# Kernel tuning notes

Measured on AMD Instinct MI355X. Metric: run time of the kernel, lower is better.

The kernel has to match this reference:

```python
import jax, jax.numpy as jnp
import numpy as np

SIGMA = 1.0
RADIUS = 3          # Gaussian kernel radius -> kernel size 7
TAU = 1.0
ITERATIONS = 20
EPS = 1e-6


def _gauss_kernel_1d(sigma: float, radius: int) -> jnp.ndarray:
    x = jnp.arange(-radius, radius + 1, dtype=jnp.float32)
    k = jnp.exp(-0.5 * (x / sigma) ** 2)
    return k / k.sum()


def _smooth(v: jnp.ndarray, k1d: jnp.ndarray) -> jnp.ndarray:
    """Separable Gaussian smoothing of a (1, C, D, H, W) field, 'same' padding."""
    C = v.shape[1]
    r = (k1d.size - 1) // 2
    for ax in range(3):
        shape = [1, 1, 1]
        shape[ax] = k1d.size
        ker = jnp.tile(k1d.reshape((1, 1) + tuple(shape)), (C, 1, 1, 1, 1))
        pad = [(r, r) if i == ax else (0, 0) for i in range(3)]
        v = jax.lax.conv_general_dilated(
            v, ker, window_strides=(1, 1, 1), padding=pad,
            dimension_numbers=('NCDHW', 'OIDHW', 'NCDHW'),
            feature_group_count=C)
    return v


def _warp(image: jnp.ndarray, disp: jnp.ndarray) -> jnp.ndarray:
    """Trilinear warp of (1,1,D,H,W) image by voxel displacement (1,3,D,H,W)."""
    D, H, W = image.shape[2:]
    gd, gh, gw = jnp.meshgrid(
        jnp.arange(D, dtype=disp.dtype),
        jnp.arange(H, dtype=disp.dtype),
        jnp.arange(W, dtype=disp.dtype), indexing='ij')
    coords = [gd + disp[0, 0], gh + disp[0, 1], gw + disp[0, 2]]
    warped = jax.scipy.ndimage.map_coordinates(image[0, 0], coords, order=1, mode='nearest')
    return warped[None, None]


def _spatial_gradient(img: jnp.ndarray) -> jnp.ndarray:
    # img: (D, H, W) -> (3, D, H, W), central differences
    return jnp.stack(jnp.gradient(img))


def _demon_forces_dual(warped, fixed, fixed_grad):
    # warped/fixed: (1,1,D,H,W); dual gradient = mean of moving/fixed gradients
    diff = (warped - fixed)[0, 0]                      # (D,H,W)
    g = 0.5 * (_spatial_gradient(warped[0, 0]) + fixed_grad)  # (3,D,H,W)
    denom = (g ** 2).sum(axis=0) + diff ** 2           # (D,H,W)
    f = jnp.where(denom > EPS, diff * g / denom, 0.0)  # (3,D,H,W)
    return f[None]                                     # (1,3,D,H,W)


def setup_inputs() -> dict:
    key = jax.random.key(0)
    k1, k2 = jax.random.split(key)
    shape = (1, 1, 128, 128, 128)
    moving_image = jax.random.uniform(k1, shape, dtype=jnp.float32)
    fixed_image = jax.random.uniform(k2, shape, dtype=jnp.float32)
    return {"moving_image": moving_image, "fixed_image": fixed_image}


def reference(moving_image, fixed_image):
    kernel = _gauss_kernel_1d(SIGMA, RADIUS)
    fixed_grad = _spatial_gradient(fixed_image[0, 0])
    vf0 = jnp.zeros((1, 3) + moving_image.shape[2:], dtype=moving_image.dtype)

    def step(vf, _):
        warped = _warp(moving_image, vf)
        forces = _demon_forces_dual(warped, fixed_image, fixed_grad)
        vf = _smooth(vf + TAU * forces, kernel)
        return vf, None

    vf, _ = jax.lax.scan(step, vf0, None, length=ITERATIONS)
    return vf
```

## Files before the change

### kernel.cpp

```cpp
#include <hip/hip_runtime.h>
#include <hip/hip_cooperative_groups.h>

namespace cg = cooperative_groups;

static constexpr int DIM = 128;
static constexpr int N = DIM * DIM * DIM;
static constexpr int ITERS = 20;
static constexpr float EPS = 1e-6f;

#define W0 0.39905028f
#define W1 0.24203624f
#define W2 0.05400559f
#define W3 0.00443305f

__device__ __forceinline__ int clamp_i(int v, int lo, int hi) {
    return min(max(v, lo), hi);
}

#define ROWS 22
#define SSTR 132
#define SC(c, r) ((((c) * ROWS) + (r)) * SSTR)
#define LDS_FLOATS (3 * ROWS * SSTR)

__device__ __forceinline__ void forces_phase(const float* __restrict__ wpd,
                                             const float* __restrict__ fix,
                                             const float* __restrict__ vf,
                                             float* __restrict__ u2,
                                             float* S, bool first, int b) {
    int z  = b >> 3;
    int y0 = (b & 7) << 4;

    for (int e = threadIdx.x; e < ROWS * 32; e += 256) {
        int x4 = e & 31;
        int r  = e >> 5;
        int gy = y0 + r - 3;
        float4 rz = make_float4(0, 0, 0, 0);
        float4 ry = make_float4(0, 0, 0, 0);
        float4 rx = make_float4(0, 0, 0, 0);
        if (gy >= 0 && gy < 128) {
            int idx = (z << 14) + (gy << 7) + (x4 << 2);
            int xb = x4 << 2;

            float4 wc4 = *(const float4*)(wpd + idx);
            float4 fc4 = *(const float4*)(fix + idx);

            int iyp = (gy < 127) ? idx + 128   : idx;
            int iym = (gy > 0)   ? idx - 128   : idx;
            int izp = (z < 127)  ? idx + 16384 : idx;
            int izm = (z > 0)    ? idx - 16384 : idx;

            float4 wyp = *(const float4*)(wpd + iyp), wym = *(const float4*)(wpd + iym);
            float4 wzp = *(const float4*)(wpd + izp), wzm = *(const float4*)(wpd + izm);
            float4 fyp = *(const float4*)(fix + iyp), fym = *(const float4*)(fix + iym);
            float4 fzp = *(const float4*)(fix + izp), fzm = *(const float4*)(fix + izm);

            float wl = __shfl_up(wc4.w, 1);
            float wr = __shfl_down(wc4.x, 1);
            float fl = __shfl_up(fc4.w, 1);
            float fr = __shfl_down(fc4.x, 1);

            float wcv[4] = {wc4.x, wc4.y, wc4.z, wc4.w};
            float fcv[4] = {fc4.x, fc4.y, fc4.z, fc4.w};
            float wypv[4] = {wyp.x, wyp.y, wyp.z, wyp.w};
            float wymv[4] = {wym.x, wym.y, wym.z, wym.w};
            float wzpv[4] = {wzp.x, wzp.y, wzp.z, wzp.w};
            float wzmv[4] = {wzm.x, wzm.y, wzm.z, wzm.w};
            float fypv[4] = {fyp.x, fyp.y, fyp.z, fyp.w};
            float fymv[4] = {fym.x, fym.y, fym.z, fym.w};
            float fzpv[4] = {fzp.x, fzp.y, fzp.z, fzp.w};
            float fzmv[4] = {fzm.x, fzm.y, fzm.z, fzm.w};

            float4 vz4 = first ? make_float4(0, 0, 0, 0) : *(const float4*)(vf + idx);
            float4 vy4 = first ? make_float4(0, 0, 0, 0) : *(const float4*)(vf + N + idx);
            float4 vx4 = first ? make_float4(0, 0, 0, 0) : *(const float4*)(vf + 2 * N + idx);
            float vzv[4] = {vz4.x, vz4.y, vz4.z, vz4.w};
            float vyv[4] = {vy4.x, vy4.y, vy4.z, vy4.w};
            float vxv[4] = {vx4.x, vx4.y, vx4.z, vx4.w};

            float ozv[4], oyv[4], oxv[4];
#pragma unroll
            for (int i = 0; i < 4; ++i) {
                float wc = wcv[i], fc = fcv[i];
                float diff = wc - fc;

                float gwz = (z == 0)   ? (wzpv[i] - wc)
                          : (z == 127) ? (wc - wzmv[i])
                          : 0.5f * (wzpv[i] - wzmv[i]);
                float gfz = (z == 0)   ? (fzpv[i] - fc)
                          : (z == 127) ? (fc - fzmv[i])
                          : 0.5f * (fzpv[i] - fzmv[i]);
                float grz = 0.5f * (gwz + gfz);

                float gwy = (gy == 0)   ? (wypv[i] - wc)
                          : (gy == 127) ? (wc - wymv[i])
                          : 0.5f * (wypv[i] - wymv[i]);
                float gfy = (gy == 0)   ? (fypv[i] - fc)
                          : (gy == 127) ? (fc - fymv[i])
                          : 0.5f * (fypv[i] - fymv[i]);
                float gry = 0.5f * (gwy + gfy);

                float wleft  = (i == 0) ? wl : wcv[i - 1];
                float wright = (i == 3) ? wr : wcv[i + 1];
                float fleft  = (i == 0) ? fl : fcv[i - 1];
                float fright = (i == 3) ? fr : fcv[i + 1];
                int xi = xb + i;
                float gwx = (xi == 0)   ? (wright - wc)
                          : (xi == 127) ? (wc - wleft)
                          : 0.5f * (wright - wleft);
                float gfx = (xi == 0)   ? (fright - fc)
                          : (xi == 127) ? (fc - fleft)
                          : 0.5f * (fright - fleft);
                float grx = 0.5f * (gwx + gfx);

                float denom = grz * grz + gry * gry + grx * grx + diff * diff;
                float s = (denom > EPS) ? (diff / denom) : 0.0f;
                ozv[i] = vzv[i] + s * grz;
                oyv[i] = vyv[i] + s * gry;
                oxv[i] = vxv[i] + s * grx;
            }
            rz = make_float4(ozv[0], ozv[1], ozv[2], ozv[3]);
            ry = make_float4(oyv[0], oyv[1], oyv[2], oyv[3]);
            rx = make_float4(oxv[0], oxv[1], oxv[2], oxv[3]);
        }

        float4 vch[3] = {rz, ry, rx};
#pragma unroll
        for (int c = 0; c < 3; ++c) {
            float4 v0 = vch[c];
            float4 m1, p1;
            m1.x = __shfl_up(v0.x, 1);  m1.y = __shfl_up(v0.y, 1);
            m1.z = __shfl_up(v0.z, 1);  m1.w = __shfl_up(v0.w, 1);
            p1.x = __shfl_down(v0.x, 1); p1.y = __shfl_down(v0.y, 1);
            p1.z = __shfl_down(v0.z, 1); p1.w = __shfl_down(v0.w, 1);
            if (x4 == 0)  m1 = make_float4(0, 0, 0, 0);
            if (x4 == 31) p1 = make_float4(0, 0, 0, 0);
            float w[12] = {m1.x, m1.y, m1.z, m1.w,
                           v0.x, v0.y, v0.z, v0.w,
                           p1.x, p1.y, p1.z, p1.w};
            float o[4];
#pragma unroll
            for (int i = 0; i < 4; ++i) {
                o[i] = W3 * (w[i + 1] + w[i + 7]) + W2 * (w[i + 2] + w[i + 6])
                     + W1 * (w[i + 3] + w[i + 5]) + W0 * w[i + 4];
            }
            *(float4*)(S + SC(c, r) + (x4 << 2)) = make_float4(o[0], o[1], o[2], o[3]);
        }
    }
    __syncthreads();

    for (int e = threadIdx.x; e < 16 * 32 * 3; e += 256) {
        int x4 = e & 31;
        int t2 = e >> 5;
        int y  = t2 & 15;
        int c  = t2 >> 4;
        const float* base = S + SC(c, y) + (x4 << 2);
        float4 v0 = *(const float4*)(base);
        float4 v1 = *(const float4*)(base + 1 * SSTR);
        float4 v2 = *(const float4*)(base + 2 * SSTR);
        float4 v3 = *(const float4*)(base + 3 * SSTR);
        float4 v4 = *(const float4*)(base + 4 * SSTR);
        float4 v5 = *(const float4*)(base + 5 * SSTR);
        float4 v6 = *(const float4*)(base + 6 * SSTR);
        float4 acc;
        acc.x = W3 * (v0.x + v6.x) + W2 * (v1.x + v5.x) + W1 * (v2.x + v4.x) + W0 * v3.x;
        acc.y = W3 * (v0.y + v6.y) + W2 * (v1.y + v5.y) + W1 * (v2.y + v4.y) + W0 * v3.y;
        acc.z = W3 * (v0.z + v6.z) + W2 * (v1.z + v5.z) + W1 * (v2.z + v4.z) + W0 * v3.z;
        acc.w = W3 * (v0.w + v6.w) + W2 * (v1.w + v5.w) + W1 * (v2.w + v4.w) + W0 * v3.w;
        *(float4*)(u2 + (size_t)c * N + ((size_t)z << 14) + ((y0 + y) << 7) + (x4 << 2)) = acc;
    }
}

__device__ __forceinline__ void zblur_phase(const float* __restrict__ u2,
                                            const float* __restrict__ mov,
                                            float* __restrict__ vf,
                                            float* __restrict__ warped,
                                            bool do_warp, int b) {
    int k  = b & 7;
    int j  = b >> 3;
    int lb = ((j & 15) << 6) + (k << 3) + (j >> 4);
    int g  = lb * 256 + threadIdx.x;
    int col = g & 16383;
    int zc  = g >> 14;
    int z0  = zc << 3;
    int x = col & 127, y = col >> 7;

    float bz[3][8];
#pragma unroll
    for (int c = 0; c < 3; ++c) {
        const float* inp = u2 + (size_t)c * N + col;
        float win[14];
#pragma unroll
        for (int i = 0; i < 14; ++i) {
            int zz = z0 - 3 + i;
            win[i] = (zz >= 0 && zz < 128) ? inp[(size_t)zz << 14] : 0.0f;
        }
#pragma unroll
        for (int k8 = 0; k8 < 8; ++k8) {
            bz[c][k8] = W3 * (win[k8] + win[k8 + 6]) + W2 * (win[k8 + 1] + win[k8 + 5])
                      + W1 * (win[k8 + 2] + win[k8 + 4]) + W0 * win[k8 + 3];
        }
        float* outp = vf + (size_t)c * N + col;
#pragma unroll
        for (int k8 = 0; k8 < 8; ++k8)
            outp[(size_t)(z0 + k8) << 14] = bz[c][k8];
    }

    if (do_warp) {
        for (int k8 = 0; k8 < 8; ++k8) {
            int z = z0 + k8;
            float cz = (float)z + bz[0][k8];
            float cy = (float)y + bz[1][k8];
            float cx = (float)x + bz[2][k8];

            float flz = floorf(cz), fly = floorf(cy), flx = floorf(cx);
            float fz = cz - flz, fy = cy - fly, fx = cx - flx;

            int zi = (int)flz, yi = (int)fly, xi = (int)flx;
            int z0c = clamp_i(zi, 0, DIM - 1), z1c = clamp_i(zi + 1, 0, DIM - 1);
            int y0c = clamp_i(yi, 0, DIM - 1), y1c = clamp_i(yi + 1, 0, DIM - 1);
            int x0c = clamp_i(xi, 0, DIM - 1), x1c = clamp_i(xi + 1, 0, DIM - 1);

            int b00 = (z0c << 14) + (y0c << 7);
            int b01 = (z0c << 14) + (y1c << 7);
            int b10 = (z1c << 14) + (y0c << 7);
            int b11 = (z1c << 14) + (y1c << 7);

            float v000 = mov[b00 + x0c], v001 = mov[b00 + x1c];
            float v010 = mov[b01 + x0c], v011 = mov[b01 + x1c];
            float v100 = mov[b10 + x0c], v101 = mov[b10 + x1c];
            float v110 = mov[b11 + x0c], v111 = mov[b11 + x1c];

            float c00 = v000 + fx * (v001 - v000);
            float c01 = v010 + fx * (v011 - v010);
            float c10 = v100 + fx * (v101 - v100);
            float c11 = v110 + fx * (v111 - v110);
            float c0 = c00 + fy * (c01 - c00);
            float c1 = c10 + fy * (c11 - c10);
            warped[((size_t)z << 14) + col] = c0 + fz * (c1 - c0);
        }
    }
}

__device__ __forceinline__ void wait_ge(unsigned int* c, unsigned int target) {
    while (__hip_atomic_load(c, __ATOMIC_ACQUIRE, __HIP_MEMORY_SCOPE_AGENT) < target)
        __builtin_amdgcn_s_sleep(1);
}

__global__ __launch_bounds__(256, 4) void demons_persistent(const float* mov,
                                                            const float* fix,
                                                            float* vf,
                                                            float* warped,
                                                            float* u2,
                                                            unsigned int* cnt) {
    cg::grid_group grid = cg::this_grid();
    __shared__ float S[LDS_FLOATS];
    int b = blockIdx.x;
    int s = b & 7;
    unsigned int* cntA = cnt;
    unsigned int* cntB = cnt + 8;

    if (b == 0 && threadIdx.x < 16) cnt[threadIdx.x] = 0u;
    grid.sync();

    for (int it = 0; it < ITERS; ++it) {
        bool first = (it == 0);
        if (!first) {
            if (threadIdx.x == 0) {
                unsigned int tgt = (unsigned int)it * 128u;
                if (s > 0) wait_ge(&cntB[s - 1], tgt);
                wait_ge(&cntB[s], tgt);
                if (s < 7) wait_ge(&cntB[s + 1], tgt);
            }
            __syncthreads();
        }
        forces_phase(first ? mov : warped, fix, vf, u2, S, first, b);
        __syncthreads();
        if (threadIdx.x == 0) {
            __hip_atomic_fetch_add(&cntA[s], 1u, __ATOMIC_RELEASE, __HIP_MEMORY_SCOPE_AGENT);
            unsigned int tgt = (unsigned int)(it + 1) * 128u;
            if (s > 0) wait_ge(&cntA[s - 1], tgt);
            wait_ge(&cntA[s], tgt);
            if (s < 7) wait_ge(&cntA[s + 1], tgt);
        }
        __syncthreads();
        zblur_phase(u2, mov, vf, warped, it < ITERS - 1, b);
        if (it < ITERS - 1) {
            __syncthreads();
            if (threadIdx.x == 0)
                __hip_atomic_fetch_add(&cntB[s], 1u, __ATOMIC_RELEASE, __HIP_MEMORY_SCOPE_AGENT);
        }
    }
}

template <bool FIRST>
__global__ __launch_bounds__(256, 4) void forces_xy_kernel(const float* __restrict__ wpd,
                                                           const float* __restrict__ fix,
                                                           const float* __restrict__ vf,
                                                           float* __restrict__ u2) {
    __shared__ float S[LDS_FLOATS];
    forces_phase(wpd, fix, vf, u2, S, FIRST, blockIdx.x);
}

template <bool DO_WARP>
__global__ __launch_bounds__(256, 4) void zblur_warp_kernel(const float* __restrict__ u2,
                                                            const float* __restrict__ mov,
                                                            float* __restrict__ vf,
                                                            float* __restrict__ warped) {
    zblur_phase(u2, mov, vf, warped, DO_WARP, blockIdx.x);
}

extern "C" void kernel_launch(void* const* d_in, const int* in_sizes, int n_in,
                              void* d_out, int out_size, void* d_ws, size_t ws_size,
                              hipStream_t stream) {
    const float* mov = (const float*)d_in[0];
    const float* fix = (const float*)d_in[1];
    float* vf = (float*)d_out;
    float* ws = (float*)d_ws;
    float* warped = ws;
    float* u2     = ws + (size_t)N;
    unsigned int* cnt = (unsigned int*)(ws + (size_t)4 * N);

    const int BLK = 256;
    const int GRID = 1024;

    static int coop_ok = -1;
    if (coop_ok < 0) {
        int dev = 0;
        (void)hipGetDevice(&dev);
        int coop = 0;
        (void)hipDeviceGetAttribute(&coop, hipDeviceAttributeCooperativeLaunch, dev);
        int ncu = 0;
        (void)hipDeviceGetAttribute(&ncu, hipDeviceAttributeMultiprocessorCount, dev);
        int occ = 0;
        (void)hipOccupancyMaxActiveBlocksPerMultiprocessor(&occ, demons_persistent, BLK, 0);
        coop_ok = (coop && (long long)occ * ncu >= GRID &&
                   ws_size >= (size_t)4 * N * sizeof(float) + 64) ? 1 : 0;
    }

    if (coop_ok) {
        void* args[] = {(void*)&mov, (void*)&fix, (void*)&vf, (void*)&warped,
                        (void*)&u2, (void*)&cnt};
        (void)hipLaunchCooperativeKernel(demons_persistent, dim3(GRID), dim3(BLK),
                                         args, 0, stream);
    } else {
        forces_xy_kernel<true><<<GRID, BLK, 0, stream>>>(mov, fix, nullptr, u2);
        zblur_warp_kernel<true><<<GRID, BLK, 0, stream>>>(u2, mov, vf, warped);
        for (int it = 1; it < ITERS - 1; ++it) {
            forces_xy_kernel<false><<<GRID, BLK, 0, stream>>>(warped, fix, vf, u2);
            zblur_warp_kernel<true><<<GRID, BLK, 0, stream>>>(u2, mov, vf, warped);
        }
        forces_xy_kernel<false><<<GRID, BLK, 0, stream>>>(warped, fix, vf, u2);
        zblur_warp_kernel<false><<<GRID, BLK, 0, stream>>>(u2, mov, vf, warped);
    }
}
```

Before: 766.9 us.

## Replace per-slab counters with fine-grained per-block dependency flags in persistent kernel

Swaps the coarse per-slab counters, each of which waited for all 128 blocks of a slab and its neighbours, for per-block flags indexed by slab and z. Each block now waits only on the neighbouring blocks whose z range its stencil or warp actually reads, with many threads polling in parallel. The aim is to cut barrier stalls and let waves of blocks proceed without full slab synchronisation. In exchange it adds more atomic polling traffic and depends on the hand-computed z dependency ranges being correct. It also adds a fallback to separate kernels when the cooperative launch fails.

Result: no change. 763.9 us (-0.4%).

```diff
diff --git a/kernel.cpp b/kernel.cpp
--- a/kernel.cpp
+++ b/kernel.cpp
@@ -251,43 +251,65 @@
                                                             float* vf,
                                                             float* warped,
                                                             float* u2,
-                                                            unsigned int* cnt) {
+                                                            unsigned int* flags) {
     cg::grid_group grid = cg::this_grid();
     __shared__ float S[LDS_FLOATS];
     int b = blockIdx.x;
     int s = b & 7;
-    unsigned int* cntA = cnt;
-    unsigned int* cntB = cnt + 8;
-
-    if (b == 0 && threadIdx.x < 16) cnt[threadIdx.x] = 0u;
+    int z = b >> 3;
+    int zc = (b >> 3) & 15;
+
+    unsigned int* flagA = flags;
+    unsigned int* flagB = flags + 1024;
+
+    if (b == 0) {
+        for (int i = threadIdx.x; i < 1024 + 128; i += 256) flags[i] = 0u;
+    }
     grid.sync();
+
+    int slo = (s > 0) ? s - 1 : 0;
+    int shi = (s < 7) ? s + 1 : 7;
+    int ns  = shi - slo + 1;
+
+    int zclo = (z >= 10) ? ((z - 10) >> 3) : 0;
+    int zchi = ((z + 3 > 127) ? 127 : (z + 3)) >> 3;
+    int ncB  = zchi - zclo + 1;
+    int totB = ns * ncB;
+
+    int plo = (zc * 8 >= 3) ? zc * 8 - 3 : 0;
+    int phi = (zc * 8 + 10 > 127) ? 127 : zc * 8 + 10;
+    int ncA = phi - plo + 1;
+    int totA = ns * ncA;
+
+    int tid = threadIdx.x;
 
     for (int it = 0; it < ITERS; ++it) {
         bool first = (it == 0);
         if (!first) {
-            if (threadIdx.x == 0) {
-                unsigned int tgt = (unsigned int)it * 128u;
-                if (s > 0) wait_ge(&cntB[s - 1], tgt);
-                wait_ge(&cntB[s], tgt);
-                if (s < 7) wait_ge(&cntB[s + 1], tgt);
+            if (tid < totB) {
+                int ss = slo + tid / ncB;
+                int c2 = zclo + tid % ncB;
+                wait_ge(&flagB[ss * 16 + c2], (unsigned int)it * 8u);
             }
             __syncthreads();
         }
         forces_phase(first ? mov : warped, fix, vf, u2, S, first, b);
         __syncthreads();
-        if (threadIdx.x == 0) {
-            __hip_atomic_fetch_add(&cntA[s], 1u, __ATOMIC_RELEASE, __HIP_MEMORY_SCOPE_AGENT);
-            unsigned int tgt = (unsigned int)(it + 1) * 128u;
-            if (s > 0) wait_ge(&cntA[s - 1], tgt);
-            wait_ge(&cntA[s], tgt);
-            if (s < 7) wait_ge(&cntA[s + 1], tgt);
+        if (tid == 0)
+            __hip_atomic_store(&flagA[s * 128 + z], (unsigned int)(it + 1),
+                               __ATOMIC_RELEASE, __HIP_MEMORY_SCOPE_AGENT);
+        if (tid < totA) {
+            int ss = slo + tid / ncA;
+            int p  = plo + tid % ncA;
+            wait_ge(&flagA[ss * 128 + p], (unsigned int)(it + 1));
         }
         __syncthreads();
         zblur_phase(u2, mov, vf, warped, it < ITERS - 1, b);
         if (it < ITERS - 1) {
             __syncthreads();
-            if (threadIdx.x == 0)
-                __hip_atomic_fetch_add(&cntB[s], 1u, __ATOMIC_RELEASE, __HIP_MEMORY_SCOPE_AGENT);
+            if (tid == 0)
+                __hip_atomic_fetch_add(&flagB[s * 16 + zc], 1u,
+                                       __ATOMIC_RELEASE, __HIP_MEMORY_SCOPE_AGENT);
         }
     }
 }
@@ -307,6 +329,19 @@
                                                             float* __restrict__ vf,
                                                             float* __restrict__ warped) {
     zblur_phase(u2, mov, vf, warped, DO_WARP, blockIdx.x);
+}
+
+static void launch_fallback(const float* mov, const float* fix, float* vf,
+                            float* warped, float* u2, hipStream_t stream) {
+    const int BLK = 256, GRID = 1024;
+    forces_xy_kernel<true><<<GRID, BLK, 0, stream>>>(mov, fix, nullptr, u2);
+    zblur_warp_kernel<true><<<GRID, BLK, 0, stream>>>(u2, mov, vf, warped);
+    for (int it = 1; it < ITERS - 1; ++it) {
+        forces_xy_kernel<false><<<GRID, BLK, 0, stream>>>(warped, fix, vf, u2);
+        zblur_warp_kernel<true><<<GRID, BLK, 0, stream>>>(u2, mov, vf, warped);
+    }
+    forces_xy_kernel<false><<<GRID, BLK, 0, stream>>>(warped, fix, vf, u2);
+    zblur_warp_kernel<false><<<GRID, BLK, 0, stream>>>(u2, mov, vf, warped);
 }
 
 extern "C" void kernel_launch(void* const* d_in, const int* in_sizes, int n_in,
@@ -318,7 +353,7 @@
     float* ws = (float*)d_ws;
     float* warped = ws;
     float* u2     = ws + (size_t)N;
-    unsigned int* cnt = (unsigned int*)(ws + (size_t)4 * N);
+    unsigned int* flags = (unsigned int*)(ws + (size_t)4 * N);
 
     const int BLK = 256;
     const int GRID = 1024;
@@ -334,22 +369,19 @@
         int occ = 0;
         (void)hipOccupancyMaxActiveBlocksPerMultiprocessor(&occ, demons_persistent, BLK, 0);
         coop_ok = (coop && (long long)occ * ncu >= GRID &&
-                   ws_size >= (size_t)4 * N * sizeof(float) + 64) ? 1 : 0;
+                   ws_size >= (size_t)4 * N * sizeof(float) + 1152 * sizeof(unsigned int)) ? 1 : 0;
     }
 
     if (coop_ok) {
         void* args[] = {(void*)&mov, (void*)&fix, (void*)&vf, (void*)&warped,
-                        (void*)&u2, (void*)&cnt};
-        (void)hipLaunchCooperativeKernel(demons_persistent, dim3(GRID), dim3(BLK),
-                                         args, 0, stream);
+                        (void*)&u2, (void*)&flags};
+        hipError_t err = hipLaunchCooperativeKernel(demons_persistent, dim3(GRID),
+                                                    dim3(BLK), args, 0, stream);
+        if (err != hipSuccess) {
+            coop_ok = 0;
+            launch_fallback(mov, fix, vf, warped, u2, stream);
+        }
     } else {
-        forces_xy_kernel<true><<<GRID, BLK, 0, stream>>>(mov, fix, nullptr, u2);
-        zblur_warp_kernel<true><<<GRID, BLK, 0, stream>>>(u2, mov, vf, warped);
-        for (int it = 1; it < ITERS - 1; ++it) {
-            forces_xy_kernel<false><<<GRID, BLK, 0, stream>>>(warped, fix, vf, u2);
-            zblur_warp_kernel<true><<<GRID, BLK, 0, stream>>>(u2, mov, vf, warped);
-        }
-        forces_xy_kernel<false><<<GRID, BLK, 0, stream>>>(warped, fix, vf, u2);
-        zblur_warp_kernel<false><<<GRID, BLK, 0, stream>>>(u2, mov, vf, warped);
-    }
-}
+        launch_fallback(mov, fix, vf, warped, u2, stream);
+    }
+}
```
